# Kernel tuning notes

Hardware: AMD Instinct MI355X
Metric: run time of the kernel (lower is better)

Reference implementation:

```python
import jax, jax.numpy as jnp
import numpy as np

B, S, DM = 4, 2048, 1024
H, HD = 16, 64  # num_heads, head_dimension


def setup_inputs() -> dict:
    key = jax.random.key(0)
    ks = jax.random.split(key, 11)
    s = 0.02
    return {
        "queries": jax.random.normal(ks[0], (B, S, DM), dtype=jnp.float32),
        "keys": jax.random.normal(ks[1], (B, S, DM), dtype=jnp.float32),
        "values": jax.random.normal(ks[2], (B, S, DM), dtype=jnp.float32),
        # projection params, stored [in, out] (transpose of torch Linear weight)
        "Wq": jax.random.normal(ks[3], (DM, H * HD), dtype=jnp.float32) * s,
        "bq": jnp.zeros((H * HD,), dtype=jnp.float32),
        "Wk": jax.random.normal(ks[4], (DM, H * HD), dtype=jnp.float32) * s,
        "bk": jnp.zeros((H * HD,), dtype=jnp.float32),
        "Wv": jax.random.normal(ks[5], (DM, H * HD), dtype=jnp.float32) * s,
        "bv": jnp.zeros((H * HD,), dtype=jnp.float32),
        "Wo": jax.random.normal(ks[6], (H * HD, DM), dtype=jnp.float32) * s,
        "bo": jnp.zeros((DM,), dtype=jnp.float32),
    }


def reference(queries, keys, values, Wq, bq, Wk, bk, Wv, bv, Wo, bo):
    b, s, _ = queries.shape
    # project and split heads: [b, s, H*HD] -> [b, H, s, HD]
    def split(x):
        return x.reshape(b, s, H, HD).transpose(0, 2, 1, 3)
    q = split(queries @ Wq + bq)
    k = split(keys @ Wk + bk)
    v = split(values @ Wv + bv)
    # raw scores [b, H, sq, sk]
    attn = jnp.einsum("bhqd,bhkd->bhqk", q, k)
    # FAITHFUL to source: mask is a no-op (masked_fill result discarded);
    # softmax over axis=2 (the QUERY axis), then scaled by 1/sqrt(HD) after.
    attn = jax.nn.softmax(attn, axis=2) / jnp.sqrt(jnp.float32(HD))
    out = jnp.einsum("bhqk,bhkd->bhqd", attn, v)  # [b, H, s, HD]
    out = out.transpose(0, 2, 1, 3).reshape(b, s, H * HD)
    return out @ Wo + bo
```

## Files before the change

### kernel.cpp

```cpp
#include <hip/hip_runtime.h>
#include <cstddef>


typedef unsigned short u16t;
typedef __attribute__((ext_vector_type(8))) short short8;
typedef __attribute__((ext_vector_type(4))) float floatx4;
typedef __attribute__((ext_vector_type(4))) unsigned int uintx4;

#define MFMA16(a, b, c) __builtin_amdgcn_mfma_f32_16x16x32_bf16((a), (b), (c), 0, 0, 0)
#define GLDS16(g, l)                                                        \
  __builtin_amdgcn_global_load_lds(                                         \
      (const __attribute__((address_space(1))) unsigned int*)(g),           \
      (__attribute__((address_space(3))) unsigned int*)(l), 16, 0, 0)

#if __has_builtin(__builtin_amdgcn_exp2f)
#define EXP2(x) __builtin_amdgcn_exp2f(x)
#else
#define EXP2(x) __expf(0.69314718f * (x))
#endif

static __device__ __forceinline__ u16t f2bf(float f) {
  union { float f; unsigned u; } v; v.f = f;
  unsigned r = v.u + 0x7FFFu + ((v.u >> 16) & 1u);
  return (u16t)(r >> 16);
}
static __device__ __forceinline__ unsigned pack2(float hi, float lo) {
  union { float f; unsigned u; } a, b; a.f = hi; b.f = lo;
  return __builtin_amdgcn_perm(a.u + 0x8000u, b.u + 0x8000u, 0x07060302u);
}
static __device__ __forceinline__ unsigned cvtpk(float lo, float hi) {
  unsigned r;
  asm("v_cvt_pk_bf16_f32 %0, %1, %2" : "=v"(r) : "v"(lo), "v"(hi));
  return r;
}

static __device__ __forceinline__ int swz(int row, int col) {
  return (((col >> 3) ^ (row & 7)) << 3) | (col & 7);
}

#define SEQ    2048
#define NHEAD  16
#define HDIM   64
#define DMODEL 1024

__global__ __launch_bounds__(256)
void wt_kernel(const float* __restrict__ W0, const float* __restrict__ W1,
               const float* __restrict__ W2, const float* __restrict__ W3,
               u16t* __restrict__ T0, u16t* __restrict__ T1,
               u16t* __restrict__ T2, u16t* __restrict__ T3) {
  int id = blockIdx.x * 256 + threadIdx.x;
  int wsel = id >> 17;
  int r = id & 131071;
  int n = r & 1023;
  int k0 = (r >> 10) << 3;
  const float* W = wsel == 0 ? W0 : wsel == 1 ? W1 : wsel == 2 ? W2 : W3;
  u16t* T = wsel == 0 ? T0 : wsel == 1 ? T1 : wsel == 2 ? T2 : T3;
  const float* src = W + (size_t)k0 * 1024 + n;
  float f[8];
#pragma unroll
  for (int i = 0; i < 8; ++i) f[i] = src[(size_t)i * 1024];
  uint4 p;
  p.x = pack2(f[1], f[0]); p.y = pack2(f[3], f[2]);
  p.z = pack2(f[5], f[4]); p.w = pack2(f[7], f[6]);
  *(uint4*)&T[(size_t)n * 1024 + (k0 & ~63) + swz(n, k0 & 63)] = p;
}

__global__ __launch_bounds__(256)
void cvt_kernel(const float* __restrict__ X, u16t* __restrict__ T) {
  int id = blockIdx.x * 256 + threadIdx.x;
  int m = id >> 7;
  int k0 = (id & 127) << 3;
  const float4* src = (const float4*)(X + (size_t)m * 1024 + k0);
  float4 a = src[0], b = src[1];
  uint4 p;
  p.x = pack2(a.y, a.x); p.y = pack2(a.w, a.z);
  p.z = pack2(b.y, b.x); p.w = pack2(b.w, b.z);
  *(uint4*)&T[(size_t)m * 1024 + (k0 & ~63) + swz(m, k0 & 63)] = p;
}

template <int MODE>
__global__ __launch_bounds__(256)
void gemm_bt(const u16t* __restrict__ Ap0, const u16t* __restrict__ Ap1,
             const u16t* __restrict__ BT0, const u16t* __restrict__ BT1,
             const float* __restrict__ bias0, const float* __restrict__ bias1,
             void* __restrict__ Cp0, void* __restrict__ Cp1,
             float sc0, float sc1, const float* __restrict__ sscv) {
  constexpr int K = 1024;
  __shared__ __align__(16) u16t lA[128 * 64];
  __shared__ __align__(16) u16t lB[128 * 64];
  const int z = blockIdx.z;
  const u16t* Ag = z ? Ap1 : Ap0;
  const u16t* BT = z ? BT1 : BT0;
  const float* bias = z ? bias1 : bias0;
  void* Cp = z ? Cp1 : Cp0;
  const float qsc = z ? sc1 : sc0;
  const int tid = threadIdx.x;
  const int lane = tid & 63, w = tid >> 6;
  const int wm = w >> 1, wn = w & 1;
  const int lrow = lane & 15, lq = lane >> 4;
  const int raw = blockIdx.y * 8 + blockIdx.x;
  const int xcd = raw & 7, slot = raw >> 3;
  const int m0 = (xcd * 8 + (slot >> 3)) * 128;
  const int n0 = (slot & 7) * 128;

  floatx4 acc[4][4];
#pragma unroll
  for (int i = 0; i < 4; ++i)
#pragma unroll
    for (int j = 0; j < 4; ++j) acc[i][j] = {0.f, 0.f, 0.f, 0.f};

  for (int kb = 0; kb < K; kb += 64) {
#pragma unroll
    for (int i = 0; i < 4; ++i) {
      int chunk = w * 4 + i;
      int off = chunk * 1024 + lane * 16;
      int r = off >> 7, ib = off & 127;
      GLDS16(Ag + (size_t)(m0 + r) * K + kb + (ib >> 1), &lA[chunk * 512]);
      GLDS16(BT + (size_t)(n0 + r) * K + kb + (ib >> 1), &lB[chunk * 512]);
    }
    __syncthreads();
#pragma unroll
    for (int kk = 0; kk < 2; ++kk) {
      short8 af[4], bfr[4];
#pragma unroll
      for (int t = 0; t < 4; ++t) {
        int ar = wm * 64 + t * 16 + lrow;
        af[t] = *(const short8*)&lA[ar * 64 + swz(ar, kk * 32 + lq * 8)];
      }
#pragma unroll
      for (int t = 0; t < 4; ++t) {
        int br = wn * 64 + t * 16 + lrow;
        bfr[t] = *(const short8*)&lB[br * 64 + swz(br, kk * 32 + lq * 8)];
      }
#pragma unroll
      for (int i = 0; i < 4; ++i)
#pragma unroll
        for (int j = 0; j < 4; ++j)
          acc[i][j] = MFMA16(af[i], bfr[j], acc[i][j]);
    }
    __syncthreads();
  }

  float bvv[4];
#pragma unroll
  for (int j = 0; j < 4; ++j) bvv[j] = bias[n0 + wn * 64 + j * 16 + lrow];
  const int h = (n0 + wn * 64) >> 6;
#pragma unroll
  for (int i = 0; i < 4; ++i) {
#pragma unroll
    for (int r = 0; r < 4; ++r) {
      int rg = m0 + wm * 64 + i * 16 + lq * 4 + r;
      int b = rg >> 11, s = rg & 2047;
      float rs;
      if constexpr (MODE == 2) rs = sscv[(size_t)(b * NHEAD + h) * SEQ + s];
      else                     rs = qsc;
#pragma unroll
      for (int j = 0; j < 4; ++j) {
        int cg = n0 + wn * 64 + j * 16 + lrow;
        float v = acc[i][j][r] + bvv[j];
        if constexpr (MODE == 1) {
          ((float*)Cp)[(size_t)rg * 1024 + cg] = v;
        } else {
          v *= rs;
          int d = cg & 63;
          size_t bh = (size_t)(b * NHEAD + h);
          if constexpr (MODE == 0) {
            ((u16t*)Cp)[(bh * SEQ + s) * HDIM + swz(s, d)] = f2bf(v);
          } else {
            int sp = (s & ~31) | (((s >> 2) & 3) << 3) | (s & 3) |
                     (((s >> 4) & 1) << 2);
            ((u16t*)Cp)[(bh * HDIM + d) * SEQ + (s & ~127) + swz(d, sp & 127)] =
                f2bf(v);
          }
        }
      }
    }
  }
}

__global__ __launch_bounds__(256)
void stats_kernel(const u16t* __restrict__ Qb, const u16t* __restrict__ Kb,
                  float* __restrict__ ss) {
  __shared__ __align__(16) u16t lK[128 * 64];
  __shared__ __align__(16) u16t lQ[128 * 64];
  const int tid = threadIdx.x, lane = tid & 63, w = tid >> 6;
  const int lrow = lane & 15, lq = lane >> 4;
  const int bh = blockIdx.x;
  const int c0 = blockIdx.y * 128;
  const u16t* Kbase = Kb + (size_t)bh * (SEQ * HDIM);
  const u16t* Qbase = Qb + (size_t)bh * (SEQ * HDIM);

#pragma unroll
  for (int i = 0; i < 4; ++i) {
    int chunk = w * 4 + i;
    GLDS16(Kbase + (size_t)c0 * HDIM + chunk * 512 + lane * 8, &lK[chunk * 512]);
  }

  short8 bfK[4];
  float lcur[2] = {0.f, 0.f};

  for (int q0 = 0; q0 < SEQ; q0 += 128) {
#pragma unroll
    for (int i = 0; i < 4; ++i) {
      int chunk = w * 4 + i;
      GLDS16(Qbase + (size_t)q0 * HDIM + chunk * 512 + lane * 8, &lQ[chunk * 512]);
    }
    __syncthreads();
    if (q0 == 0) {
#pragma unroll
      for (int nt = 0; nt < 2; ++nt) {
        int kr = w * 32 + nt * 16 + lrow;
        bfK[nt * 2]     = *(const short8*)&lK[kr * 64 + swz(kr, lq * 8)];
        bfK[nt * 2 + 1] = *(const short8*)&lK[kr * 64 + swz(kr, lq * 8 + 32)];
      }
    }
#pragma unroll
    for (int mt = 0; mt < 8; ++mt) {
      int qr = mt * 16 + lrow;
      short8 af0 = *(const short8*)&lQ[qr * 64 + swz(qr, lq * 8)];
      short8 af1 = *(const short8*)&lQ[qr * 64 + swz(qr, lq * 8 + 32)];
#pragma unroll
      for (int nt = 0; nt < 2; ++nt) {
        floatx4 a = {0.f, 0.f, 0.f, 0.f};
        a = MFMA16(af0, bfK[nt * 2], a);
        a = MFMA16(af1, bfK[nt * 2 + 1], a);
        lcur[nt] += EXP2(a[0]) + EXP2(a[1]) + EXP2(a[2]) + EXP2(a[3]);
      }
    }
    __syncthreads();
  }
#pragma unroll
  for (int t = 0; t < 2; ++t) {
    float ll = lcur[t];
    ll += __shfl_xor(ll, 16);
    ll += __shfl_xor(ll, 32);
    lcur[t] = ll;
  }
  if (lane < 16) {
#pragma unroll
    for (int t = 0; t < 2; ++t) {
      int col = c0 + w * 32 + t * 16 + lane;
      ss[(size_t)bh * SEQ + col] = 1.f / (8.f * lcur[t]);
    }
  }
}

__global__ __launch_bounds__(256, 2)
void attn_kernel(const u16t* __restrict__ Qb, const u16t* __restrict__ Kb,
                 const u16t* __restrict__ Vt, u16t* __restrict__ Hout) {
  __shared__ __align__(16) u16t sK[2][8192];
  __shared__ __align__(16) u16t sV[2][8192];
  const int tid = threadIdx.x, lane = tid & 63, w = tid >> 6;
  const int lrow = lane & 15, lq = lane >> 4;
  const int bh = blockIdx.x, q0 = blockIdx.y * 256;
  const size_t hb = (size_t)bh * (SEQ * HDIM);

  auto stage = [&](int t) {
    u16t* dK = sK[t & 1];
    u16t* dV = sV[t & 1];
    const int k0 = t << 7;
#pragma unroll
    for (int i = 0; i < 4; ++i) {
      int chunk = w * 4 + i;
      GLDS16(Kb + hb + (size_t)k0 * HDIM + chunk * 512 + lane * 8, &dK[chunk * 512]);
    }
#pragma unroll
    for (int i = 0; i < 4; ++i) {
      int chunk = w * 4 + i;
      int off = chunk * 1024 + lane * 16;
      int d = off >> 8, ib = off & 255;
      GLDS16(Vt + hb + ((size_t)d << 11) + k0 + (ib >> 1), &dV[chunk * 512]);
    }
  };
  auto loadK = [&](short8 dst[2][2], const u16t* K_, int kw) {
#pragma unroll
    for (int t = 0; t < 2; ++t) {
      int kr = (kw * 2 + t) * 16 + lrow;
      dst[t][0] = *(const short8*)&K_[kr * 64 + swz(kr, lq * 8)];
      dst[t][1] = *(const short8*)&K_[kr * 64 + swz(kr, lq * 8 + 32)];
    }
  };
  auto loadV = [&](short8 dst[4], const u16t* V_, int kw) {
#pragma unroll
    for (int dt = 0; dt < 4; ++dt) {
      int vr = dt * 16 + lrow;
      dst[dt] = *(const short8*)&V_[vr * 128 + swz(vr, kw * 32 + lq * 8)];
    }
  };

  u16t* qs = (u16t*)sK;
#pragma unroll
  for (int i = 0; i < 8; ++i) {
    int chunk = w * 8 + i;
    GLDS16(Qb + hb + (size_t)q0 * HDIM + chunk * 512 + lane * 8, &qs[chunk * 512]);
  }
  __syncthreads();
  short8 bq[4][2];
#pragma unroll
  for (int j = 0; j < 4; ++j) {
    int qr = w * 64 + j * 16 + lrow;
    bq[j][0] = *(const short8*)&qs[qr * 64 + swz(qr, lq * 8)];
    bq[j][1] = *(const short8*)&qs[qr * 64 + swz(qr, lq * 8 + 32)];
  }
  __syncthreads();

  auto qk = [&](const short8 ak[2][2], floatx4 s[4][2]) {
    __builtin_amdgcn_s_setprio(1);
#pragma unroll
    for (int j = 0; j < 4; ++j) {
      floatx4 a = {0.f, 0.f, 0.f, 0.f}, b = {0.f, 0.f, 0.f, 0.f};
      a = MFMA16(ak[0][0], bq[j][0], a);
      a = MFMA16(ak[0][1], bq[j][1], a);
      b = MFMA16(ak[1][0], bq[j][0], b);
      b = MFMA16(ak[1][1], bq[j][1], b);
      s[j][0] = a; s[j][1] = b;
    }
    __builtin_amdgcn_s_setprio(0);
  };
  auto ep = [&](const floatx4 s[4][2], short8 pa[4]) {
#pragma unroll
    for (int j = 0; j < 4; ++j) {
      uintx4 pw;
      pw[0] = cvtpk(EXP2(s[j][0][0]), EXP2(s[j][0][1]));
      pw[1] = cvtpk(EXP2(s[j][0][2]), EXP2(s[j][0][3]));
      pw[2] = cvtpk(EXP2(s[j][1][0]), EXP2(s[j][1][1]));
      pw[3] = cvtpk(EXP2(s[j][1][2]), EXP2(s[j][1][3]));
      pa[j] = __builtin_bit_cast(short8, pw);
    }
  };

  floatx4 ao[4][4];
#pragma unroll
  for (int j = 0; j < 4; ++j)
#pragma unroll
    for (int t = 0; t < 4; ++t) ao[j][t] = {0.f, 0.f, 0.f, 0.f};

  stage(0);
  stage(1);

#pragma unroll 2
  for (int kt = 0; kt < 16; ++kt) {
    if (kt < 15) asm volatile("s_waitcnt vmcnt(8)" ::: "memory");
    else         asm volatile("s_waitcnt vmcnt(0)" ::: "memory");
    __builtin_amdgcn_s_barrier();
    const u16t* K_ = sK[kt & 1];
    const u16t* V_ = sV[kt & 1];

    short8 ak0[2][2];
    loadK(ak0, K_, 0);
    floatx4 s0[4][2];
    qk(ak0, s0);
    short8 pa[4];
    ep(s0, pa);

#pragma unroll
    for (int kw = 0; kw < 4; ++kw) {
      short8 bv[4];
      loadV(bv, V_, kw);
      short8 akN[2][2];
      floatx4 sN[4][2];
      if (kw < 3) {
        loadK(akN, K_, kw + 1);
        qk(akN, sN);
      }
      __builtin_amdgcn_s_setprio(1);
#pragma unroll
      for (int dt = 0; dt < 4; ++dt)
#pragma unroll
        for (int j = 0; j < 4; ++j)
          ao[j][dt] = MFMA16(pa[j], bv[dt], ao[j][dt]);
      __builtin_amdgcn_s_setprio(0);
      if (kw < 3) {
        short8 paN[4];
        ep(sN, paN);
#pragma unroll
        for (int j = 0; j < 4; ++j) pa[j] = paN[j];
      }
    }

    asm volatile("s_waitcnt lgkmcnt(0)" ::: "memory");
    __builtin_amdgcn_s_barrier();
    if (kt < 14) stage(kt + 2);
  }

  const int b = bh >> 4, h = bh & 15;
#pragma unroll
  for (int j = 0; j < 4; ++j)
#pragma unroll
    for (int dt = 0; dt < 4; ++dt) {
      int d = dt * 16 + lrow;
#pragma unroll
      for (int r = 0; r < 4; ++r) {
        int q = q0 + w * 64 + j * 16 + lq * 4 + r;
        Hout[((size_t)b * SEQ + q) * DMODEL + h * HDIM + swz(q, d)] = f2bf(ao[j][dt][r]);
      }
    }
}

extern "C" void kernel_launch(void* const* d_in, const int* in_sizes, int n_in,
                              void* d_out, int out_size, void* d_ws, size_t ws_size,
                              hipStream_t stream) {
  (void)in_sizes; (void)n_in; (void)out_size; (void)ws_size;
  const float* queries = (const float*)d_in[0];
  const float* keys    = (const float*)d_in[1];
  const float* values  = (const float*)d_in[2];
  const float* Wq = (const float*)d_in[3];
  const float* bq = (const float*)d_in[4];
  const float* Wk = (const float*)d_in[5];
  const float* bk = (const float*)d_in[6];
  const float* Wv = (const float*)d_in[7];
  const float* bv = (const float*)d_in[8];
  const float* Wo = (const float*)d_in[9];
  const float* bo = (const float*)d_in[10];

  char* ws = (char*)d_ws;
  const size_t MB = 1024 * 1024;
  u16t* Qb   = (u16t*)(ws + 0 * MB);
  u16t* Kb   = (u16t*)(ws + 16 * MB);
  u16t* qcv  = (u16t*)(ws + 32 * MB);
  u16t* vcv  = qcv;
  u16t* Hout = qcv;
  u16t* kcv  = (u16t*)(ws + 48 * MB);
  u16t* Vt   = kcv;
  u16t* wqt  = (u16t*)(ws + 64 * MB);
  u16t* wkt  = (u16t*)(ws + 66 * MB);
  u16t* wvt  = (u16t*)(ws + 68 * MB);
  u16t* wot  = (u16t*)(ws + 70 * MB);
  float* ssc = (float*)(ws + 72 * MB);

  wt_kernel<<<2048, 256, 0, stream>>>(Wq, Wk, Wv, Wo, wqt, wkt, wvt, wot);

  cvt_kernel<<<4096, 256, 0, stream>>>(queries, qcv);
  cvt_kernel<<<4096, 256, 0, stream>>>(keys, kcv);

  gemm_bt<0><<<dim3(8, 64, 2), 256, 0, stream>>>(
      qcv, kcv, wqt, wkt, bq, bk, Qb, Kb, 1.44269504f, 1.0f, nullptr);

  cvt_kernel<<<4096, 256, 0, stream>>>(values, vcv);

  stats_kernel<<<dim3(64, 16), 256, 0, stream>>>(Qb, Kb, ssc);

  gemm_bt<2><<<dim3(8, 64, 1), 256, 0, stream>>>(
      vcv, vcv, wvt, wvt, bv, bv, Vt, Vt, 1.0f, 1.0f, ssc);

  attn_kernel<<<dim3(64, 8), 256, 0, stream>>>(Qb, Kb, Vt, Hout);

  gemm_bt<1><<<dim3(8, 64, 1), 256, 0, stream>>>(
      Hout, Hout, wot, wot, bo, bo, d_out, d_out, 1.0f, 1.0f, nullptr);
}
```

Before: 377.4 us.

## Double-buffer GEMM LDS tiles with async prefetch and merge Q/K conversion launches

The projection GEMM now keeps two LDS buffers per operand and issues global-to-LDS loads two k-steps ahead. It uses explicit vmcnt waits and raw barriers so loads overlap with MFMA work, and raises wave priority around the MFMA block. The two fp32-to-bf16 conversion launches for queries and keys are merged into one kernel. This aims to hide global load latency in the GEMMs and cut one launch, at the cost of doubling LDS per block (64KB), which may reduce occupancy.

```diff
diff --git a/kernel.cpp b/kernel.cpp
--- a/kernel.cpp
+++ b/kernel.cpp
@@ -66,6 +66,24 @@
 }
 
 __global__ __launch_bounds__(256)
+void cvt2_kernel(const float* __restrict__ X0, const float* __restrict__ X1,
+                 u16t* __restrict__ T0, u16t* __restrict__ T1) {
+  int id = blockIdx.x * 256 + threadIdx.x;
+  int wsel = id >> 20;
+  int r = id & 1048575;
+  int m = r >> 7;
+  int k0 = (r & 127) << 3;
+  const float* X = wsel == 0 ? X0 : X1;
+  u16t* T = wsel == 0 ? T0 : T1;
+  const float4* src = (const float4*)(X + (size_t)m * 1024 + k0);
+  float4 a = src[0], b = src[1];
+  uint4 p;
+  p.x = pack2(a.y, a.x); p.y = pack2(a.w, a.z);
+  p.z = pack2(b.y, b.x); p.w = pack2(b.w, b.z);
+  *(uint4*)&T[(size_t)m * 1024 + (k0 & ~63) + swz(m, k0 & 63)] = p;
+}
+
+__global__ __launch_bounds__(256)
 void cvt_kernel(const float* __restrict__ X, u16t* __restrict__ T) {
   int id = blockIdx.x * 256 + threadIdx.x;
   int m = id >> 7;
@@ -86,8 +104,8 @@
              void* __restrict__ Cp0, void* __restrict__ Cp1,
              float sc0, float sc1, const float* __restrict__ sscv) {
   constexpr int K = 1024;
-  __shared__ __align__(16) u16t lA[128 * 64];
-  __shared__ __align__(16) u16t lB[128 * 64];
+  __shared__ __align__(16) u16t lA[2][128 * 64];
+  __shared__ __align__(16) u16t lB[2][128 * 64];
   const int z = blockIdx.z;
   const u16t* Ag = z ? Ap1 : Ap0;
   const u16t* BT = z ? BT1 : BT0;
@@ -103,42 +121,59 @@
   const int m0 = (xcd * 8 + (slot >> 3)) * 128;
   const int n0 = (slot & 7) * 128;
 
-  floatx4 acc[4][4];
-#pragma unroll
-  for (int i = 0; i < 4; ++i)
-#pragma unroll
-    for (int j = 0; j < 4; ++j) acc[i][j] = {0.f, 0.f, 0.f, 0.f};
-
-  for (int kb = 0; kb < K; kb += 64) {
+  auto stage = [&](int t) {
+    const int kb = t << 6;
+    u16t* dA = lA[t & 1];
+    u16t* dB = lB[t & 1];
 #pragma unroll
     for (int i = 0; i < 4; ++i) {
       int chunk = w * 4 + i;
       int off = chunk * 1024 + lane * 16;
       int r = off >> 7, ib = off & 127;
-      GLDS16(Ag + (size_t)(m0 + r) * K + kb + (ib >> 1), &lA[chunk * 512]);
-      GLDS16(BT + (size_t)(n0 + r) * K + kb + (ib >> 1), &lB[chunk * 512]);
-    }
-    __syncthreads();
+      GLDS16(Ag + (size_t)(m0 + r) * K + kb + (ib >> 1), &dA[chunk * 512]);
+      GLDS16(BT + (size_t)(n0 + r) * K + kb + (ib >> 1), &dB[chunk * 512]);
+    }
+  };
+
+  floatx4 acc[4][4];
+#pragma unroll
+  for (int i = 0; i < 4; ++i)
+#pragma unroll
+    for (int j = 0; j < 4; ++j) acc[i][j] = {0.f, 0.f, 0.f, 0.f};
+
+  stage(0);
+  stage(1);
+
+  for (int t = 0; t < 16; ++t) {
+    if (t < 15) asm volatile("s_waitcnt vmcnt(8)" ::: "memory");
+    else        asm volatile("s_waitcnt vmcnt(0)" ::: "memory");
+    __builtin_amdgcn_s_barrier();
+    const u16t* A_ = lA[t & 1];
+    const u16t* B_ = lB[t & 1];
 #pragma unroll
     for (int kk = 0; kk < 2; ++kk) {
       short8 af[4], bfr[4];
 #pragma unroll
-      for (int t = 0; t < 4; ++t) {
-        int ar = wm * 64 + t * 16 + lrow;
-        af[t] = *(const short8*)&lA[ar * 64 + swz(ar, kk * 32 + lq * 8)];
-      }
-#pragma unroll
-      for (int t = 0; t < 4; ++t) {
-        int br = wn * 64 + t * 16 + lrow;
-        bfr[t] = *(const short8*)&lB[br * 64 + swz(br, kk * 32 + lq * 8)];
-      }
+      for (int tt = 0; tt < 4; ++tt) {
+        int ar = wm * 64 + tt * 16 + lrow;
+        af[tt] = *(const short8*)&A_[ar * 64 + swz(ar, kk * 32 + lq * 8)];
+      }
+#pragma unroll
+      for (int tt = 0; tt < 4; ++tt) {
+        int br = wn * 64 + tt * 16 + lrow;
+        bfr[tt] = *(const short8*)&B_[br * 64 + swz(br, kk * 32 + lq * 8)];
+      }
+      __builtin_amdgcn_s_setprio(1);
 #pragma unroll
       for (int i = 0; i < 4; ++i)
 #pragma unroll
         for (int j = 0; j < 4; ++j)
           acc[i][j] = MFMA16(af[i], bfr[j], acc[i][j]);
-    }
-    __syncthreads();
+      __builtin_amdgcn_s_setprio(0);
+    }
+    asm volatile("s_waitcnt lgkmcnt(0)" ::: "memory");
+    __builtin_amdgcn_s_barrier();
+    if (t < 14) stage(t + 2);
   }
 
   float bvv[4];
@@ -430,8 +465,7 @@
 
   wt_kernel<<<2048, 256, 0, stream>>>(Wq, Wk, Wv, Wo, wqt, wkt, wvt, wot);
 
-  cvt_kernel<<<4096, 256, 0, stream>>>(queries, qcv);
-  cvt_kernel<<<4096, 256, 0, stream>>>(keys, kcv);
+  cvt2_kernel<<<8192, 256, 0, stream>>>(queries, keys, qcv, kcv);
 
   gemm_bt<0><<<dim3(8, 64, 2), 256, 0, stream>>>(
       qcv, kcv, wqt, wkt, bq, bk, Qb, Kb, 1.44269504f, 1.0f, nullptr);
```

After: 381.2 us. No clear change (+1.0%).

## Fuse fp32-to-bf16 conversion into QKV projection and fold softmax norm into scores

Applied to the files above, without the earlier changes.

Removes the three separate cvt kernels by loading fp32 activations directly in the projection GEMM, packing them to bf16 and storing into LDS, then runs Q, K and V projections in one launch. The per-key softmax normalizer is now kept as a log2 offset that is staged into LDS and used as the MFMA accumulator initial value in the attention kernel, so it no longer scales V in the V projection. This removes intermediate bf16 activation round trips and a couple of launches. In exchange, the A-operand loads become synchronous scalar fp32 loads in the GEMM inner loop instead of async global-to-LDS copies, which may stall the main loop.

```diff
diff --git a/kernel.cpp b/kernel.cpp
--- a/kernel.cpp
+++ b/kernel.cpp
@@ -12,6 +12,10 @@
   __builtin_amdgcn_global_load_lds(                                         \
       (const __attribute__((address_space(1))) unsigned int*)(g),           \
       (__attribute__((address_space(3))) unsigned int*)(l), 16, 0, 0)
+#define GLDS4(g, l)                                                         \
+  __builtin_amdgcn_global_load_lds(                                         \
+      (const __attribute__((address_space(1))) unsigned int*)(g),           \
+      (__attribute__((address_space(3))) unsigned int*)(l), 4, 0, 0)
 
 #if __has_builtin(__builtin_amdgcn_exp2f)
 #define EXP2(x) __builtin_amdgcn_exp2f(x)
@@ -66,34 +70,22 @@
 }
 
 __global__ __launch_bounds__(256)
-void cvt_kernel(const float* __restrict__ X, u16t* __restrict__ T) {
-  int id = blockIdx.x * 256 + threadIdx.x;
-  int m = id >> 7;
-  int k0 = (id & 127) << 3;
-  const float4* src = (const float4*)(X + (size_t)m * 1024 + k0);
-  float4 a = src[0], b = src[1];
-  uint4 p;
-  p.x = pack2(a.y, a.x); p.y = pack2(a.w, a.z);
-  p.z = pack2(b.y, b.x); p.w = pack2(b.w, b.z);
-  *(uint4*)&T[(size_t)m * 1024 + (k0 & ~63) + swz(m, k0 & 63)] = p;
-}
-
-template <int MODE>
-__global__ __launch_bounds__(256)
-void gemm_bt(const u16t* __restrict__ Ap0, const u16t* __restrict__ Ap1,
-             const u16t* __restrict__ BT0, const u16t* __restrict__ BT1,
-             const float* __restrict__ bias0, const float* __restrict__ bias1,
-             void* __restrict__ Cp0, void* __restrict__ Cp1,
-             float sc0, float sc1, const float* __restrict__ sscv) {
+void proj_kernel(const float* __restrict__ Qf, const float* __restrict__ Kf,
+                 const float* __restrict__ Vf,
+                 const u16t* __restrict__ WQ, const u16t* __restrict__ WK,
+                 const u16t* __restrict__ WV,
+                 const float* __restrict__ bq, const float* __restrict__ bk,
+                 const float* __restrict__ bv,
+                 u16t* __restrict__ Qb, u16t* __restrict__ Kb,
+                 u16t* __restrict__ Vt) {
   constexpr int K = 1024;
   __shared__ __align__(16) u16t lA[128 * 64];
   __shared__ __align__(16) u16t lB[128 * 64];
   const int z = blockIdx.z;
-  const u16t* Ag = z ? Ap1 : Ap0;
-  const u16t* BT = z ? BT1 : BT0;
-  const float* bias = z ? bias1 : bias0;
-  void* Cp = z ? Cp1 : Cp0;
-  const float qsc = z ? sc1 : sc0;
+  const float* Ag = z == 0 ? Qf : z == 1 ? Kf : Vf;
+  const u16t* BT = z == 0 ? WQ : z == 1 ? WK : WV;
+  const float* bias = z == 0 ? bq : z == 1 ? bk : bv;
+  const float qsc = z == 0 ? 1.44269504f : 1.0f;
   const int tid = threadIdx.x;
   const int lane = tid & 63, w = tid >> 6;
   const int wm = w >> 1, wn = w & 1;
@@ -111,11 +103,20 @@
 
   for (int kb = 0; kb < K; kb += 64) {
 #pragma unroll
+    for (int i = 0; i < 8; ++i) {
+      int e = (i * 256 + tid) * 4;
+      int r = e >> 6, c = e & 63;
+      const float* src = Ag + (size_t)(m0 + r) * K + kb + c;
+      uint2 p;
+      p.x = pack2(src[1], src[0]);
+      p.y = pack2(src[3], src[2]);
+      *(uint2*)&lA[r * 64 + swz(r, c)] = p;
+    }
+#pragma unroll
     for (int i = 0; i < 4; ++i) {
       int chunk = w * 4 + i;
       int off = chunk * 1024 + lane * 16;
       int r = off >> 7, ib = off & 127;
-      GLDS16(Ag + (size_t)(m0 + r) * K + kb + (ib >> 1), &lA[chunk * 512]);
       GLDS16(BT + (size_t)(n0 + r) * K + kb + (ib >> 1), &lB[chunk * 512]);
     }
     __syncthreads();
@@ -145,33 +146,25 @@
 #pragma unroll
   for (int j = 0; j < 4; ++j) bvv[j] = bias[n0 + wn * 64 + j * 16 + lrow];
   const int h = (n0 + wn * 64) >> 6;
+  u16t* Out = z == 0 ? Qb : Kb;
 #pragma unroll
   for (int i = 0; i < 4; ++i) {
 #pragma unroll
     for (int r = 0; r < 4; ++r) {
       int rg = m0 + wm * 64 + i * 16 + lq * 4 + r;
       int b = rg >> 11, s = rg & 2047;
-      float rs;
-      if constexpr (MODE == 2) rs = sscv[(size_t)(b * NHEAD + h) * SEQ + s];
-      else                     rs = qsc;
+      size_t bh = (size_t)(b * NHEAD + h);
 #pragma unroll
       for (int j = 0; j < 4; ++j) {
         int cg = n0 + wn * 64 + j * 16 + lrow;
+        int d = cg & 63;
         float v = acc[i][j][r] + bvv[j];
-        if constexpr (MODE == 1) {
-          ((float*)Cp)[(size_t)rg * 1024 + cg] = v;
+        if (z < 2) {
+          Out[(bh * SEQ + s) * HDIM + swz(s, d)] = f2bf(v * qsc);
         } else {
-          v *= rs;
-          int d = cg & 63;
-          size_t bh = (size_t)(b * NHEAD + h);
-          if constexpr (MODE == 0) {
-            ((u16t*)Cp)[(bh * SEQ + s) * HDIM + swz(s, d)] = f2bf(v);
-          } else {
-            int sp = (s & ~31) | (((s >> 2) & 3) << 3) | (s & 3) |
-                     (((s >> 4) & 1) << 2);
-            ((u16t*)Cp)[(bh * HDIM + d) * SEQ + (s & ~127) + swz(d, sp & 127)] =
-                f2bf(v);
-          }
+          int sp = (s & ~31) | (((s >> 2) & 3) << 3) | (s & 3) |
+                   (((s >> 4) & 1) << 2);
+          Vt[(bh * HDIM + d) * SEQ + (s & ~127) + swz(d, sp & 127)] = f2bf(v);
         }
       }
     }
@@ -180,7 +173,7 @@
 
 __global__ __launch_bounds__(256)
 void stats_kernel(const u16t* __restrict__ Qb, const u16t* __restrict__ Kb,
-                  float* __restrict__ ss) {
+                  float* __restrict__ lss) {
   __shared__ __align__(16) u16t lK[128 * 64];
   __shared__ __align__(16) u16t lQ[128 * 64];
   const int tid = threadIdx.x, lane = tid & 63, w = tid >> 6;
@@ -240,24 +233,28 @@
 #pragma unroll
     for (int t = 0; t < 2; ++t) {
       int col = c0 + w * 32 + t * 16 + lane;
-      ss[(size_t)bh * SEQ + col] = 1.f / (8.f * lcur[t]);
+      lss[(size_t)bh * SEQ + col] = -3.0f - __log2f(lcur[t]);
     }
   }
 }
 
 __global__ __launch_bounds__(256, 2)
 void attn_kernel(const u16t* __restrict__ Qb, const u16t* __restrict__ Kb,
-                 const u16t* __restrict__ Vt, u16t* __restrict__ Hout) {
+                 const u16t* __restrict__ Vt, const float* __restrict__ Lb,
+                 u16t* __restrict__ Hout) {
   __shared__ __align__(16) u16t sK[2][8192];
   __shared__ __align__(16) u16t sV[2][8192];
+  __shared__ __align__(16) float sL[2][128];
   const int tid = threadIdx.x, lane = tid & 63, w = tid >> 6;
   const int lrow = lane & 15, lq = lane >> 4;
   const int bh = blockIdx.x, q0 = blockIdx.y * 256;
   const size_t hb = (size_t)bh * (SEQ * HDIM);
+  const float* Lg = Lb + (size_t)bh * SEQ;
 
   auto stage = [&](int t) {
     u16t* dK = sK[t & 1];
     u16t* dV = sV[t & 1];
+    float* dL = sL[t & 1];
     const int k0 = t << 7;
 #pragma unroll
     for (int i = 0; i < 4; ++i) {
@@ -271,6 +268,8 @@
       int d = off >> 8, ib = off & 255;
       GLDS16(Vt + hb + ((size_t)d << 11) + k0 + (ib >> 1), &dV[chunk * 512]);
     }
+    GLDS4(Lg + k0 + lane, &dL[0]);
+    GLDS4(Lg + k0 + 64 + lane, &dL[64]);
   };
   auto loadK = [&](short8 dst[2][2], const u16t* K_, int kw) {
 #pragma unroll
@@ -304,11 +303,11 @@
   }
   __syncthreads();
 
-  auto qk = [&](const short8 ak[2][2], floatx4 s[4][2]) {
+  auto qk = [&](const short8 ak[2][2], floatx4 s[4][2], floatx4 cA, floatx4 cB) {
     __builtin_amdgcn_s_setprio(1);
 #pragma unroll
     for (int j = 0; j < 4; ++j) {
-      floatx4 a = {0.f, 0.f, 0.f, 0.f}, b = {0.f, 0.f, 0.f, 0.f};
+      floatx4 a = cA, b = cB;
       a = MFMA16(ak[0][0], bq[j][0], a);
       a = MFMA16(ak[0][1], bq[j][1], a);
       b = MFMA16(ak[1][0], bq[j][0], b);
@@ -340,16 +339,19 @@
 
 #pragma unroll 2
   for (int kt = 0; kt < 16; ++kt) {
-    if (kt < 15) asm volatile("s_waitcnt vmcnt(8)" ::: "memory");
+    if (kt < 15) asm volatile("s_waitcnt vmcnt(10)" ::: "memory");
     else         asm volatile("s_waitcnt vmcnt(0)" ::: "memory");
     __builtin_amdgcn_s_barrier();
     const u16t* K_ = sK[kt & 1];
     const u16t* V_ = sV[kt & 1];
+    const float* L_ = sL[kt & 1];
 
     short8 ak0[2][2];
     loadK(ak0, K_, 0);
+    floatx4 cA = *(const floatx4*)&L_[lq * 4];
+    floatx4 cB = *(const floatx4*)&L_[16 + lq * 4];
     floatx4 s0[4][2];
-    qk(ak0, s0);
+    qk(ak0, s0, cA, cB);
     short8 pa[4];
     ep(s0, pa);
 
@@ -361,7 +363,9 @@
       floatx4 sN[4][2];
       if (kw < 3) {
         loadK(akN, K_, kw + 1);
-        qk(akN, sN);
+        floatx4 cAn = *(const floatx4*)&L_[(kw + 1) * 32 + lq * 4];
+        floatx4 cBn = *(const floatx4*)&L_[(kw + 1) * 32 + 16 + lq * 4];
+        qk(akN, sN, cAn, cBn);
       }
       __builtin_amdgcn_s_setprio(1);
 #pragma unroll
@@ -395,6 +399,76 @@
         Hout[((size_t)b * SEQ + q) * DMODEL + h * HDIM + swz(q, d)] = f2bf(ao[j][dt][r]);
       }
     }
+}
+
+__global__ __launch_bounds__(256)
+void outproj_kernel(const u16t* __restrict__ Ag, const u16t* __restrict__ BT,
+                    const float* __restrict__ bias, float* __restrict__ Cp) {
+  constexpr int K = 1024;
+  __shared__ __align__(16) u16t lA[128 * 64];
+  __shared__ __align__(16) u16t lB[128 * 64];
+  const int tid = threadIdx.x;
+  const int lane = tid & 63, w = tid >> 6;
+  const int wm = w >> 1, wn = w & 1;
+  const int lrow = lane & 15, lq = lane >> 4;
+  const int raw = blockIdx.y * 8 + blockIdx.x;
+  const int xcd = raw & 7, slot = raw >> 3;
+  const int m0 = (xcd * 8 + (slot >> 3)) * 128;
+  const int n0 = (slot & 7) * 128;
+
+  floatx4 acc[4][4];
+#pragma unroll
+  for (int i = 0; i < 4; ++i)
+#pragma unroll
+    for (int j = 0; j < 4; ++j) acc[i][j] = {0.f, 0.f, 0.f, 0.f};
+
+  for (int kb = 0; kb < K; kb += 64) {
+#pragma unroll
+    for (int i = 0; i < 4; ++i) {
+      int chunk = w * 4 + i;
+      int off = chunk * 1024 + lane * 16;
+      int r = off >> 7, ib = off & 127;
+      GLDS16(Ag + (size_t)(m0 + r) * K + kb + (ib >> 1), &lA[chunk * 512]);
+      GLDS16(BT + (size_t)(n0 + r) * K + kb + (ib >> 1), &lB[chunk * 512]);
+    }
+    __syncthreads();
+#pragma unroll
+    for (int kk = 0; kk < 2; ++kk) {
+      short8 af[4], bfr[4];
+#pragma unroll
+      for (int t = 0; t < 4; ++t) {
+        int ar = wm * 64 + t * 16 + lrow;
+        af[t] = *(const short8*)&lA[ar * 64 + swz(ar, kk * 32 + lq * 8)];
+      }
+#pragma unroll
+      for (int t = 0; t < 4; ++t) {
+        int br = wn * 64 + t * 16 + lrow;
+        bfr[t] = *(const short8*)&lB[br * 64 + swz(br, kk * 32 + lq * 8)];
+      }
+#pragma unroll
+      for (int i = 0; i < 4; ++i)
+#pragma unroll
+        for (int j = 0; j < 4; ++j)
+          acc[i][j] = MFMA16(af[i], bfr[j], acc[i][j]);
+    }
+    __syncthreads();
+  }
+
+  float bvv[4];
+#pragma unroll
+  for (int j = 0; j < 4; ++j) bvv[j] = bias[n0 + wn * 64 + j * 16 + lrow];
+#pragma unroll
+  for (int i = 0; i < 4; ++i) {
+#pragma unroll
+    for (int r = 0; r < 4; ++r) {
+      int rg = m0 + wm * 64 + i * 16 + lq * 4 + r;
+#pragma unroll
+      for (int j = 0; j < 4; ++j) {
+        int cg = n0 + wn * 64 + j * 16 + lrow;
+        Cp[(size_t)rg * 1024 + cg] = acc[i][j][r] + bvv[j];
+      }
+    }
+  }
 }
 
 extern "C" void kernel_launch(void* const* d_in, const int* in_sizes, int n_in,
@@ -417,34 +491,22 @@
   const size_t MB = 1024 * 1024;
   u16t* Qb   = (u16t*)(ws + 0 * MB);
   u16t* Kb   = (u16t*)(ws + 16 * MB);
-  u16t* qcv  = (u16t*)(ws + 32 * MB);
-  u16t* vcv  = qcv;
-  u16t* Hout = qcv;
-  u16t* kcv  = (u16t*)(ws + 48 * MB);
-  u16t* Vt   = kcv;
+  u16t* Hout = (u16t*)(ws + 32 * MB);
+  u16t* Vt   = (u16t*)(ws + 48 * MB);
   u16t* wqt  = (u16t*)(ws + 64 * MB);
   u16t* wkt  = (u16t*)(ws + 66 * MB);
   u16t* wvt  = (u16t*)(ws + 68 * MB);
   u16t* wot  = (u16t*)(ws + 70 * MB);
-  float* ssc = (float*)(ws + 72 * MB);
+  float* lss = (float*)(ws + 72 * MB);
 
   wt_kernel<<<2048, 256, 0, stream>>>(Wq, Wk, Wv, Wo, wqt, wkt, wvt, wot);
 
-  cvt_kernel<<<4096, 256, 0, stream>>>(queries, qcv);
-  cvt_kernel<<<4096, 256, 0, stream>>>(keys, kcv);
-
-  gemm_bt<0><<<dim3(8, 64, 2), 256, 0, stream>>>(
-      qcv, kcv, wqt, wkt, bq, bk, Qb, Kb, 1.44269504f, 1.0f, nullptr);
-
-  cvt_kernel<<<4096, 256, 0, stream>>>(values, vcv);
-
-  stats_kernel<<<dim3(64, 16), 256, 0, stream>>>(Qb, Kb, ssc);
-
-  gemm_bt<2><<<dim3(8, 64, 1), 256, 0, stream>>>(
-      vcv, vcv, wvt, wvt, bv, bv, Vt, Vt, 1.0f, 1.0f, ssc);
-
-  attn_kernel<<<dim3(64, 8), 256, 0, stream>>>(Qb, Kb, Vt, Hout);
-
-  gemm_bt<1><<<dim3(8, 64, 1), 256, 0, stream>>>(
-      Hout, Hout, wot, wot, bo, bo, d_out, d_out, 1.0f, 1.0f, nullptr);
-}
+  proj_kernel<<<dim3(8, 64, 3), 256, 0, stream>>>(
+      queries, keys, values, wqt, wkt, wvt, bq, bk, bv, Qb, Kb, Vt);
+
+  stats_kernel<<<dim3(64, 16), 256, 0, stream>>>(Qb, Kb, lss);
+
+  attn_kernel<<<dim3(64, 8), 256, 0, stream>>>(Qb, Kb, Vt, lss, Hout);
+
+  outproj_kernel<<<dim3(8, 64), 256, 0, stream>>>(Hout, wot, bo, (float*)d_out);
+}
```

Result: no change. 378.6 us (+0.3%).
